# Performance work log

Measured on AMD Instinct MI355X. Metric: run time of the kernel, lower is better.

The kernel has to match this reference:

```python
import jax, jax.numpy as jnp
import numpy as np

EPS = 1e-5
QMAX = 127.0   # 8-bit symmetric: representable range [-128, 127]
QMIN = -128.0


def ste_round(x):
    # straight-through rounding (identity gradient)
    return x + jax.lax.stop_gradient(jnp.round(x) - x)


def setup_inputs() -> dict:
    key = jax.random.key(0)
    ks = jax.random.split(key, 7)
    N, C_in, C_out, H, W = 64, 256, 128, 56, 56
    x = jax.random.normal(ks[0], (N, C_in, H, W), jnp.float32)
    act_scaling_factor = jax.random.uniform(ks[1], (1,), jnp.float32, 0.02, 0.08)
    bn_weight = 1.0 + 0.3 * jax.random.normal(ks[2], (C_in,), jnp.float32)
    bn_bias = 0.1 * jax.random.normal(ks[3], (C_in,), jnp.float32)
    bn_mean = 0.1 * jax.random.normal(ks[4], (C_in,), jnp.float32)
    bn_var = jax.random.uniform(ks[5], (C_in,), jnp.float32, 0.5, 1.5)
    conv_weight = 0.05 * jax.random.normal(ks[6], (C_out, C_in, 1, 1), jnp.float32)
    return {
        "x": x,
        "act_scaling_factor": act_scaling_factor,
        "bn_weight": bn_weight,
        "bn_bias": bn_bias,
        "bn_mean": bn_mean,
        "bn_var": bn_var,
        "conv_weight": conv_weight,
    }


def _fwd(x, act_scaling_factor, bn_weight, bn_bias, bn_mean, bn_var, conv_weight):
    act_sf = act_scaling_factor.reshape(())

    # ---- QuantBn: fold BN, quantize folded scale per-channel (8-bit symmetric) ----
    inv_std = jax.lax.rsqrt(bn_var + EPS)
    scale = bn_weight * inv_std                    # [C_in]
    shift = bn_bias - bn_mean * scale              # [C_in]
    bn_sf = jnp.max(jnp.abs(scale)) / QMAX         # per-tensor bn weight scale
    scale_q = jnp.clip(ste_round(scale / bn_sf), QMIN, QMAX) * bn_sf
    bias_sf = bn_sf * act_sf                        # bias quantized at combined scale
    shift_q = ste_round(shift / bias_sf) * bias_sf
    x = x * scale_q[None, :, None, None] + shift_q[None, :, None, None]

    # ---- ReLU ----
    x = jnp.maximum(x, 0.0)

    # ---- QuantAct 1: per-tensor symmetric 8-bit requant ----
    sf1 = jnp.max(jnp.abs(x)) / QMAX
    x = jnp.clip(ste_round(x / sf1), QMIN, QMAX) * sf1

    # ---- QuantConv2d: per-output-channel 8-bit symmetric weight quant, 1x1 conv ----
    w_sf = jnp.max(jnp.abs(conv_weight), axis=(1, 2, 3)) / QMAX   # [C_out]
    w_q = jnp.clip(ste_round(conv_weight / w_sf[:, None, None, None]), QMIN, QMAX) \
          * w_sf[:, None, None, None]
    y = jax.lax.conv_general_dilated(
        x, w_q, window_strides=(1, 1), padding='VALID',
        dimension_numbers=('NCHW', 'OIHW', 'NCHW'))

    # ---- QuantAct 2 ----
    sf2 = jnp.max(jnp.abs(y)) / QMAX
    y = jnp.clip(ste_round(y / sf2), QMIN, QMAX) * sf2

    # ---- QuantAveragePool2d (2x2, stride 2): average in integer domain, re-round ----
    N, C, H, W = y.shape
    y_int = (y / sf2).reshape(N, C, H // 2, 2, W // 2, 2).mean(axis=(3, 5))
    out = ste_round(y_int) * sf2
    return out, sf2


def reference(x, act_scaling_factor, bn_weight, bn_bias, bn_mean, bn_var, conv_weight):
    return _fwd(x, act_scaling_factor, bn_weight, bn_bias, bn_mean, bn_var, conv_weight)
```

## Files before the change

kernel.cpp:

```cpp
#include <hip/hip_runtime.h>

#define QMAXF 127.0f

typedef _Float16 f16x4 __attribute__((ext_vector_type(4)));
typedef float f32x4 __attribute__((ext_vector_type(4)));
typedef int i32x4 __attribute__((ext_vector_type(4)));

__global__ __launch_bounds__(256) void k0_prep(
    const float* __restrict__ actsf, const float* __restrict__ bnw,
    const float* __restrict__ bnb, const float* __restrict__ bnm,
    const float* __restrict__ bnv, const float* __restrict__ cw,
    float* __restrict__ wsf, float* __restrict__ scq, float* __restrict__ shq,
    unsigned short* __restrict__ wq16, signed char* __restrict__ wq8,
    unsigned int* __restrict__ gmax) {
  const int t = threadIdx.x;
  __shared__ float red[4];
  float scale, shift;
  {
#pragma clang fp contract(off)
    float inv = 1.0f / sqrtf(bnv[t] + 1e-5f);
    scale = bnw[t] * inv;
    float tmp = bnm[t] * scale;
    shift = bnb[t] - tmp;
  }
  float a = fabsf(scale);
  for (int o = 32; o > 0; o >>= 1) a = fmaxf(a, __shfl_xor(a, o));
  if ((t & 63) == 0) red[t >> 6] = a;
  __syncthreads();
  const float amax = fmaxf(fmaxf(red[0], red[1]), fmaxf(red[2], red[3]));
  const float bn_sf = amax / QMAXF;
  scq[t] = fminf(fmaxf(rintf(scale / bn_sf), -128.f), 127.f) * bn_sf;
  const float bias_sf = bn_sf * actsf[0];
  shq[t] = rintf(shift / bias_sf) * bias_sf;
  if (t == 0) *gmax = 0u;
  const int r = t >> 1, half = t & 1;
  const float4* wrow = (const float4*)(cw + r * 256 + half * 128);
  float mx = 0.f;
#pragma unroll
  for (int j = 0; j < 32; ++j) {
    const float4 v = wrow[j];
    mx = fmaxf(mx, fmaxf(fmaxf(fabsf(v.x), fabsf(v.y)), fmaxf(fabsf(v.z), fabsf(v.w))));
  }
  mx = fmaxf(mx, __shfl_xor(mx, 1));
  const float wsf_v = mx / QMAXF;
  if (half == 0) wsf[r] = wsf_v;
  unsigned* w16w = (unsigned*)wq16;
  int* w8w = (int*)wq8;
#pragma unroll
  for (int j = 0; j < 32; ++j) {
    const float4 v = wrow[j];
    const float q0 = fminf(fmaxf(rintf(v.x / wsf_v), -128.f), 127.f);
    const float q1 = fminf(fmaxf(rintf(v.y / wsf_v), -128.f), 127.f);
    const float q2 = fminf(fmaxf(rintf(v.z / wsf_v), -128.f), 127.f);
    const float q3 = fminf(fmaxf(rintf(v.w / wsf_v), -128.f), 127.f);
    w8w[r * 64 + half * 32 + j] =
        ((int)q0 & 255) | (((int)q1 & 255) << 8) | (((int)q2 & 255) << 16) | (((int)q3 & 255) << 24);
    const unsigned h0 = __builtin_bit_cast(unsigned short, (_Float16)q0);
    const unsigned h1 = __builtin_bit_cast(unsigned short, (_Float16)q1);
    const unsigned h2 = __builtin_bit_cast(unsigned short, (_Float16)q2);
    const unsigned h3 = __builtin_bit_cast(unsigned short, (_Float16)q3);
    w16w[r * 128 + half * 64 + 2 * j]     = h0 | (h1 << 16);
    w16w[r * 128 + half * 64 + 2 * j + 1] = h2 | (h3 << 16);
  }
}

__global__ __launch_bounds__(256) void k1_max(
    const float* __restrict__ x, const float* __restrict__ scq,
    const float* __restrict__ shq, unsigned int* __restrict__ gmax) {
  const int t = threadIdx.x;
  const int b = blockIdx.x;
  const int n = b >> 5, cg = b & 31;
  __shared__ float red[4];
  const float4* __restrict__ x4 = (const float4*)x + (long)(n * 256 + cg * 8) * 784;
  float m = 0.f;
  for (int r = 0; r < 8; ++r) {
    const float s = scq[cg * 8 + r], sh = shq[cg * 8 + r];
    const float4* row = x4 + r * 784;
    for (int j = t; j < 784; j += 256) {
      const float4 v = row[j];
      float z0, z1, z2, z3;
      {
#pragma clang fp contract(off)
        z0 = v.x * s + sh; z1 = v.y * s + sh; z2 = v.z * s + sh; z3 = v.w * s + sh;
      }
      m = fmaxf(m, fmaxf(fmaxf(z0, z1), fmaxf(z2, z3)));
    }
  }
  for (int o = 32; o > 0; o >>= 1) m = fmaxf(m, __shfl_xor(m, o));
  if ((t & 63) == 0) red[t >> 6] = m;
  __syncthreads();
  if (t == 0) {
    const float mm = fmaxf(fmaxf(red[0], red[1]), fmaxf(red[2], red[3]));
    atomicMax(gmax, __float_as_uint(mm));
  }
}

__global__ __launch_bounds__(256, 2) void k2f_quant_gemm(
    const float* __restrict__ x, const float* __restrict__ scq,
    const float* __restrict__ shq, const unsigned int* __restrict__ gmax,
    const signed char* __restrict__ wq8, const float* __restrict__ wsf,
    signed char* __restrict__ xqT, float* __restrict__ blockmax) {
  __shared__ int sw[112 * 64];
  __shared__ float comax[128];
  __shared__ float red2[4];
  const int t = threadIdx.x, w = t >> 6, l = t & 63, m = l & 15, g = l >> 4;
  const int blk = blockIdx.x, n = blk / 28, tt = blk - n * 28;
  const float sf1 = __uint_as_float(*gmax) / QMAXF;
  const float* __restrict__ xb = x + (long)n * 802816 + tt * 112;

  for (int it = 0; it < 2; ++it) {
    const int task = it * 256 + t;
    if (task < 448) {
      const int slot = task & 15, hwq = task >> 4;
      const int hw0 = hwq * 4, ci0 = slot * 16;
      int wbuf[4][4] = {{0, 0, 0, 0}, {0, 0, 0, 0}, {0, 0, 0, 0}, {0, 0, 0, 0}};
#pragma unroll
      for (int j = 0; j < 16; ++j) {
        const float4 v = *(const float4*)(xb + (long)(ci0 + j) * 3136 + hw0);
        const float s = scq[ci0 + j], sh = shq[ci0 + j];
        float z0, z1, z2, z3;
        {
#pragma clang fp contract(off)
          z0 = v.x * s + sh; z1 = v.y * s + sh; z2 = v.z * s + sh; z3 = v.w * s + sh;
        }
        const float q0 = fminf(fmaxf(rintf(fmaxf(z0, 0.f) / sf1), -128.f), 127.f);
        const float q1 = fminf(fmaxf(rintf(fmaxf(z1, 0.f) / sf1), -128.f), 127.f);
        const float q2 = fminf(fmaxf(rintf(fmaxf(z2, 0.f) / sf1), -128.f), 127.f);
        const float q3 = fminf(fmaxf(rintf(fmaxf(z3, 0.f) / sf1), -128.f), 127.f);
        wbuf[0][j >> 2] |= ((int)q0 & 255) << ((j & 3) * 8);
        wbuf[1][j >> 2] |= ((int)q1 & 255) << ((j & 3) * 8);
        wbuf[2][j >> 2] |= ((int)q2 & 255) << ((j & 3) * 8);
        wbuf[3][j >> 2] |= ((int)q3 & 255) << ((j & 3) * 8);
      }
#pragma unroll
      for (int dh = 0; dh < 4; ++dh) {
        const int hw = hw0 + dh;
        *(i32x4*)&sw[hw * 64 + ((slot ^ (hw & 7)) << 2)] = *(const i32x4*)wbuf[dh];
      }
    }
  }
  __syncthreads();

  signed char* __restrict__ dst = xqT + ((long)(n * 3136 + tt * 112)) * 256;
  for (int it = 0; it < 7; ++it) {
    const int idx = it * 256 + t;
    const int hw = idx >> 4, c = idx & 15;
    const i32x4 v = *(const i32x4*)&sw[hw * 64 + ((c ^ (hw & 7)) << 2)];
    *(i32x4*)(dst + hw * 256 + c * 16) = v;
  }

  i32x4 wf[2][4];
#pragma unroll
  for (int ct = 0; ct < 2; ++ct)
#pragma unroll
    for (int ks = 0; ks < 4; ++ks)
      wf[ct][ks] = *(const i32x4*)(wq8 + (w * 32 + ct * 16 + m) * 256 + ks * 64 + g * 16);

  i32x4 acc[2][7];
#pragma unroll
  for (int ct = 0; ct < 2; ++ct)
#pragma unroll
    for (int ht = 0; ht < 7; ++ht) acc[ct][ht] = (i32x4){0, 0, 0, 0};

#pragma unroll
  for (int ks = 0; ks < 4; ++ks) {
    i32x4 xf[7];
#pragma unroll
    for (int ht = 0; ht < 7; ++ht) {
      const int row = ht * 16 + m;
      xf[ht] = *(const i32x4*)&sw[row * 64 + (((ks * 4 + g) ^ (row & 7)) << 2)];
    }
#pragma unroll
    for (int ct = 0; ct < 2; ++ct)
#pragma unroll
      for (int ht = 0; ht < 7; ++ht)
        acc[ct][ht] = __builtin_amdgcn_mfma_i32_16x16x64_i8(wf[ct][ks], xf[ht], acc[ct][ht], 0, 0, 0);
  }

  int im[2][4];
#pragma unroll
  for (int ct = 0; ct < 2; ++ct)
#pragma unroll
    for (int r = 0; r < 4; ++r) {
      int v = 0;
#pragma unroll
      for (int ht = 0; ht < 7; ++ht) {
        int a = acc[ct][ht][r];
        a = a < 0 ? -a : a;
        v = a > v ? a : v;
      }
      im[ct][r] = v;
    }
#pragma unroll
  for (int o = 1; o < 16; o <<= 1)
#pragma unroll
    for (int ct = 0; ct < 2; ++ct)
#pragma unroll
      for (int r = 0; r < 4; ++r) {
        const int other = __shfl_xor(im[ct][r], o);
        im[ct][r] = other > im[ct][r] ? other : im[ct][r];
      }
  if (m == 0) {
#pragma unroll
    for (int ct = 0; ct < 2; ++ct)
#pragma unroll
      for (int r = 0; r < 4; ++r)
        comax[w * 32 + ct * 16 + g * 4 + r] = (float)im[ct][r];
  }
  __syncthreads();
  float v = 0.f;
  if (t < 128) v = comax[t] * (sf1 * wsf[t]);
  for (int o = 32; o > 0; o >>= 1) v = fmaxf(v, __shfl_xor(v, o));
  if ((t & 63) == 0) red2[t >> 6] = v;
  __syncthreads();
  if (t == 0)
    blockmax[blk] = fmaxf(fmaxf(red2[0], red2[1]), fmaxf(red2[2], red2[3]));
}

__global__ __launch_bounds__(256) void k2b_sf2(
    const float* __restrict__ blockmax, float* __restrict__ sf2slot,
    float* __restrict__ outsf2) {
  const int t = threadIdx.x;
  __shared__ float red[4];
  float m = 0.f;
  for (int i = t; i < 1792; i += 256) m = fmaxf(m, blockmax[i]);
  for (int o = 32; o > 0; o >>= 1) m = fmaxf(m, __shfl_xor(m, o));
  if ((t & 63) == 0) red[t >> 6] = m;
  __syncthreads();
  if (t == 0) {
    const float sf2 = fmaxf(fmaxf(red[0], red[1]), fmaxf(red[2], red[3])) / QMAXF;
    sf2slot[0] = sf2;
    outsf2[0] = sf2;
  }
}

__global__ __launch_bounds__(256) void k3_final(
    const signed char* __restrict__ xqT, const signed char* __restrict__ wq8,
    const float* __restrict__ wsf, const unsigned int* __restrict__ gmax,
    const float* __restrict__ sf2p, float* __restrict__ out) {
  __shared__ _Float16 q2[128 * 116];
  const int t = threadIdx.x, w = t >> 6, l = t & 63;
  const int m = l & 15, g = l >> 4;
  const int blk = blockIdx.x;
  const int n = blk / 28, tt = blk - n * 28;
  const float sf1 = __uint_as_float(*gmax) / QMAXF;
  const signed char* __restrict__ xb = xqT + ((long)(n * 3136 + tt * 112)) * 256;

  i32x4 wf[2][4];
#pragma unroll
  for (int ct = 0; ct < 2; ++ct)
#pragma unroll
    for (int ks = 0; ks < 4; ++ks)
      wf[ct][ks] = *(const i32x4*)(wq8 + (w * 32 + ct * 16 + m) * 256 + ks * 64 + g * 16);

  i32x4 acc[2][7];
#pragma unroll
  for (int ct = 0; ct < 2; ++ct)
#pragma unroll
    for (int ht = 0; ht < 7; ++ht) acc[ct][ht] = (i32x4){0, 0, 0, 0};

#pragma unroll
  for (int ks = 0; ks < 4; ++ks) {
    i32x4 xf[7];
#pragma unroll
    for (int ht = 0; ht < 7; ++ht)
      xf[ht] = *(const i32x4*)(xb + (ht * 16 + m) * 256 + ks * 64 + g * 16);
#pragma unroll
    for (int ct = 0; ct < 2; ++ct)
#pragma unroll
      for (int ht = 0; ht < 7; ++ht)
        acc[ct][ht] = __builtin_amdgcn_mfma_i32_16x16x64_i8(wf[ct][ks], xf[ht], acc[ct][ht], 0, 0, 0);
  }

  const float sf2 = sf2p[0];
  float fac[2][4];
#pragma unroll
  for (int ct = 0; ct < 2; ++ct)
#pragma unroll
    for (int r = 0; r < 4; ++r)
      fac[ct][r] = sf1 * wsf[w * 32 + ct * 16 + g * 4 + r];
#pragma unroll
  for (int ct = 0; ct < 2; ++ct)
#pragma unroll
    for (int ht = 0; ht < 7; ++ht)
#pragma unroll
      for (int r = 0; r < 4; ++r) {
        const float y = (float)acc[ct][ht][r] * fac[ct][r];
        const float q = fminf(fmaxf(rintf(y / sf2), -128.f), 127.f);
        q2[(w * 32 + ct * 16 + g * 4 + r) * 116 + ht * 16 + m] = (_Float16)q;
      }
  __syncthreads();
  const long obase = (long)n * 100352 + tt * 28;
  for (int i = t; i < 3584; i += 256) {
    const unsigned co = (unsigned)i / 28u;
    const unsigned wo = (unsigned)i - co * 28u;
    const _Float16* row = q2 + co * 116;
    const float a = (float)row[2 * wo] + (float)row[2 * wo + 1] +
                    (float)row[56 + 2 * wo] + (float)row[56 + 2 * wo + 1];
    out[obase + (long)co * 784 + wo] = rintf(a * 0.25f) * sf2;
  }
}

union K2Smem {
  float xq[112][132];
  float q2[128][113];
  float comax[128];
};

template <bool FINAL>
__global__ __launch_bounds__(256, 2) void k2_gemm(
    const float* __restrict__ x, const float* __restrict__ scq,
    const float* __restrict__ shq, const unsigned short* __restrict__ wqu,
    const float* __restrict__ wsf, const unsigned int* __restrict__ gmax1,
    const float* __restrict__ sf2p, float* __restrict__ blockmax,
    float* __restrict__ out) {
  __shared__ K2Smem sm;
  __shared__ float red2[4];
  const int t = threadIdx.x;
  const int w = t >> 6;
  const int l = t & 63;
  const int blk = blockIdx.x;
  const int n = blk / 28;
  const int tt = blk - n * 28;
  const long xbase = (long)n * 802816 + tt * 112;
  const float sf1 = __uint_as_float(*gmax1) / QMAXF;
  const _Float16* __restrict__ wq16 = (const _Float16*)wqu;
  f32x4 acc[2][7];
#pragma unroll
  for (int ct = 0; ct < 2; ++ct)
#pragma unroll
    for (int ht = 0; ht < 7; ++ht) acc[ct][ht] = (f32x4){0.f, 0.f, 0.f, 0.f};

  for (int phase = 0; phase < 2; ++phase) {
    for (int it = 0; it < 14; ++it) {
      const unsigned f = (unsigned)t + (unsigned)it * 256u;
      const unsigned ci_l = f / 28u;
      const unsigned hwp = (f - ci_l * 28u) * 4u;
      const int ci = phase * 128 + (int)ci_l;
      const float4 v = *(const float4*)(x + xbase + (long)ci * 3136 + hwp);
      const float s = scq[ci], sh = shq[ci];
      float z0, z1, z2, z3;
      {
#pragma clang fp contract(off)
        z0 = v.x * s + sh; z1 = v.y * s + sh; z2 = v.z * s + sh; z3 = v.w * s + sh;
      }
      z0 = fmaxf(z0, 0.f); z1 = fmaxf(z1, 0.f); z2 = fmaxf(z2, 0.f); z3 = fmaxf(z3, 0.f);
      sm.xq[hwp + 0][ci_l] = fminf(fmaxf(rintf(z0 / sf1), -128.f), 127.f);
      sm.xq[hwp + 1][ci_l] = fminf(fmaxf(rintf(z1 / sf1), -128.f), 127.f);
      sm.xq[hwp + 2][ci_l] = fminf(fmaxf(rintf(z2 / sf1), -128.f), 127.f);
      sm.xq[hwp + 3][ci_l] = fminf(fmaxf(rintf(z3 / sf1), -128.f), 127.f);
    }
    __syncthreads();
    const int kw = ((l >> 4) << 2);
#pragma unroll
    for (int ks = 0; ks < 8; ++ks) {
      const int kb = ks * 16 + kw;
      f16x4 xf[7];
#pragma unroll
      for (int ht = 0; ht < 7; ++ht) {
        const float4 xv = *(const float4*)&sm.xq[ht * 16 + (l & 15)][kb];
        f16x4 h;
        h[0] = (_Float16)xv.x; h[1] = (_Float16)xv.y;
        h[2] = (_Float16)xv.z; h[3] = (_Float16)xv.w;
        xf[ht] = h;
      }
#pragma unroll
      for (int ct = 0; ct < 2; ++ct) {
        const int co = (w << 5) + (ct << 4) + (l & 15);
        const f16x4 wfv = *(const f16x4*)(wq16 + co * 256 + phase * 128 + kb);
#pragma unroll
        for (int ht = 0; ht < 7; ++ht)
          acc[ct][ht] = __builtin_amdgcn_mfma_f32_16x16x16f16(wfv, xf[ht], acc[ct][ht], 0, 0, 0);
      }
    }
    __syncthreads();
  }

  const int g = (l >> 4);
  if (!FINAL) {
    float im[2][4];
#pragma unroll
    for (int ct = 0; ct < 2; ++ct)
#pragma unroll
      for (int r = 0; r < 4; ++r) {
        float v = 0.f;
#pragma unroll
        for (int ht = 0; ht < 7; ++ht) v = fmaxf(v, fabsf(acc[ct][ht][r]));
        im[ct][r] = v;
      }
#pragma unroll
    for (int o = 1; o < 16; o <<= 1)
#pragma unroll
      for (int ct = 0; ct < 2; ++ct)
#pragma unroll
        for (int r = 0; r < 4; ++r)
          im[ct][r] = fmaxf(im[ct][r], __shfl_xor(im[ct][r], o));
    if ((l & 15) == 0) {
#pragma unroll
      for (int ct = 0; ct < 2; ++ct)
#pragma unroll
        for (int r = 0; r < 4; ++r)
          sm.comax[(w << 5) + (ct << 4) + (g << 2) + r] = im[ct][r];
    }
    __syncthreads();
    float v = 0.f;
    if (t < 128) v = sm.comax[t] * (sf1 * wsf[t]);
    for (int o = 32; o > 0; o >>= 1) v = fmaxf(v, __shfl_xor(v, o));
    if ((t & 63) == 0) red2[t >> 6] = v;
    __syncthreads();
    if (t == 0)
      blockmax[blk] = fmaxf(fmaxf(red2[0], red2[1]), fmaxf(red2[2], red2[3]));
  } else {
    const float sf2 = sf2p[0];
    float fac[2][4];
#pragma unroll
    for (int ct = 0; ct < 2; ++ct)
#pragma unroll
      for (int r = 0; r < 4; ++r)
        fac[ct][r] = sf1 * wsf[(w << 5) + (ct << 4) + (g << 2) + r];
#pragma unroll
    for (int ct = 0; ct < 2; ++ct)
#pragma unroll
      for (int ht = 0; ht < 7; ++ht)
#pragma unroll
        for (int r = 0; r < 4; ++r) {
          const float y = acc[ct][ht][r] * fac[ct][r];
          const float q = fminf(fmaxf(rintf(y / sf2), -128.f), 127.f);
          sm.q2[(w << 5) + (ct << 4) + (g << 2) + r][ht * 16 + (l & 15)] = q;
        }
    __syncthreads();
    const long obase = (long)n * 100352 + tt * 28;
    for (int i = t; i < 3584; i += 256) {
      const unsigned co = (unsigned)i / 28u;
      const unsigned wo = (unsigned)i - co * 28u;
      const float a = sm.q2[co][2 * wo];
      const float b = sm.q2[co][2 * wo + 1];
      const float c = sm.q2[co][56 + 2 * wo];
      const float d = sm.q2[co][56 + 2 * wo + 1];
      const float avg = (a + b + c + d) * 0.25f;
      out[obase + (long)co * 784 + wo] = rintf(avg) * sf2;
    }
  }
}

extern "C" void kernel_launch(void* const* d_in, const int* in_sizes, int n_in,
                              void* d_out, int out_size, void* d_ws, size_t ws_size,
                              hipStream_t stream) {
  const float* x     = (const float*)d_in[0];
  const float* actsf = (const float*)d_in[1];
  const float* bnw   = (const float*)d_in[2];
  const float* bnb   = (const float*)d_in[3];
  const float* bnm   = (const float*)d_in[4];
  const float* bnv   = (const float*)d_in[5];
  const float* cw    = (const float*)d_in[6];
  float* out = (float*)d_out;
  char* ws = (char*)d_ws;

  unsigned int* gmax  = (unsigned int*)ws;
  float* sf2slot      = (float*)(ws + 8);
  float* scq          = (float*)(ws + 1024);
  float* shq          = (float*)(ws + 2048);
  float* wsf          = (float*)(ws + 3072);
  signed char* wq8    = (signed char*)(ws + 4096);
  unsigned short* wq16= (unsigned short*)(ws + 36864);
  float* blockmax     = (float*)(ws + 102400);
  signed char* xqT    = (signed char*)(ws + 131072);
  const size_t NEED = 131072ull + 64ull * 3136ull * 256ull;

  hipLaunchKernelGGL(k0_prep, dim3(1), dim3(256), 0, stream,
                     actsf, bnw, bnb, bnm, bnv, cw, wsf, scq, shq, wq16, wq8, gmax);
  hipLaunchKernelGGL(k1_max, dim3(2048), dim3(256), 0, stream, x, scq, shq, gmax);
  if (ws_size >= NEED) {
    hipLaunchKernelGGL(k2f_quant_gemm, dim3(1792), dim3(256), 0, stream,
                       x, scq, shq, gmax, wq8, wsf, xqT, blockmax);
    hipLaunchKernelGGL(k2b_sf2, dim3(1), dim3(256), 0, stream,
                       blockmax, sf2slot, out + (out_size - 1));
    hipLaunchKernelGGL(k3_final, dim3(1792), dim3(256), 0, stream,
                       xqT, wq8, wsf, gmax, sf2slot, out);
  } else {
    hipLaunchKernelGGL(HIP_KERNEL_NAME(k2_gemm<false>), dim3(1792), dim3(256), 0, stream,
                       x, scq, shq, wq16, wsf, gmax, sf2slot, blockmax, out);
    hipLaunchKernelGGL(k2b_sf2, dim3(1), dim3(256), 0, stream,
                       blockmax, sf2slot, out + (out_size - 1));
    hipLaunchKernelGGL(HIP_KERNEL_NAME(k2_gemm<true>), dim3(1792), dim3(256), 0, stream,
                       x, scq, shq, wq16, wsf, gmax, sf2slot, blockmax, out);
  }
}
```

Before: 171.9 us.

## Shrink quant-GEMM tiles, fold sf2 reduction into final kernel, drop fp16 path

The quantize+GEMM pass now uses 64-pixel tiles (3136 blocks) with a smaller LDS buffer and per-iteration weight loads, targeting higher occupancy (launch bounds 4). The separate single-block sf2 reduction kernel is removed: every block of the final kernel re-reduces the 3136 block maxima itself, saving one launch but adding redundant reads. Weight fragments are loaded inside the loop instead of kept in registers to cut register pressure. The fp16 fallback path, used when the workspace was too small, is deleted along with its weight buffer.

```diff
diff --git a/kernel.cpp b/kernel.cpp
--- a/kernel.cpp
+++ b/kernel.cpp
@@ -2,7 +2,6 @@
 
 #define QMAXF 127.0f
 
-typedef _Float16 f16x4 __attribute__((ext_vector_type(4)));
 typedef float f32x4 __attribute__((ext_vector_type(4)));
 typedef int i32x4 __attribute__((ext_vector_type(4)));
 
@@ -11,8 +10,7 @@
     const float* __restrict__ bnb, const float* __restrict__ bnm,
     const float* __restrict__ bnv, const float* __restrict__ cw,
     float* __restrict__ wsf, float* __restrict__ scq, float* __restrict__ shq,
-    unsigned short* __restrict__ wq16, signed char* __restrict__ wq8,
-    unsigned int* __restrict__ gmax) {
+    signed char* __restrict__ wq8, unsigned int* __restrict__ gmax) {
   const int t = threadIdx.x;
   __shared__ float red[4];
   float scale, shift;
@@ -44,7 +42,6 @@
   mx = fmaxf(mx, __shfl_xor(mx, 1));
   const float wsf_v = mx / QMAXF;
   if (half == 0) wsf[r] = wsf_v;
-  unsigned* w16w = (unsigned*)wq16;
   int* w8w = (int*)wq8;
 #pragma unroll
   for (int j = 0; j < 32; ++j) {
@@ -55,12 +52,6 @@
     const float q3 = fminf(fmaxf(rintf(v.w / wsf_v), -128.f), 127.f);
     w8w[r * 64 + half * 32 + j] =
         ((int)q0 & 255) | (((int)q1 & 255) << 8) | (((int)q2 & 255) << 16) | (((int)q3 & 255) << 24);
-    const unsigned h0 = __builtin_bit_cast(unsigned short, (_Float16)q0);
-    const unsigned h1 = __builtin_bit_cast(unsigned short, (_Float16)q1);
-    const unsigned h2 = __builtin_bit_cast(unsigned short, (_Float16)q2);
-    const unsigned h3 = __builtin_bit_cast(unsigned short, (_Float16)q3);
-    w16w[r * 128 + half * 64 + 2 * j]     = h0 | (h1 << 16);
-    w16w[r * 128 + half * 64 + 2 * j + 1] = h2 | (h3 << 16);
   }
 }
 
@@ -95,86 +86,76 @@
   }
 }
 
-__global__ __launch_bounds__(256, 2) void k2f_quant_gemm(
+__global__ __launch_bounds__(256, 4) void k2f_quant_gemm(
     const float* __restrict__ x, const float* __restrict__ scq,
     const float* __restrict__ shq, const unsigned int* __restrict__ gmax,
     const signed char* __restrict__ wq8, const float* __restrict__ wsf,
     signed char* __restrict__ xqT, float* __restrict__ blockmax) {
-  __shared__ int sw[112 * 64];
+  __shared__ int sw[64 * 64];
   __shared__ float comax[128];
   __shared__ float red2[4];
   const int t = threadIdx.x, w = t >> 6, l = t & 63, m = l & 15, g = l >> 4;
-  const int blk = blockIdx.x, n = blk / 28, tt = blk - n * 28;
+  const int blk = blockIdx.x, n = blk / 49, tt = blk - n * 49;
   const float sf1 = __uint_as_float(*gmax) / QMAXF;
-  const float* __restrict__ xb = x + (long)n * 802816 + tt * 112;
-
-  for (int it = 0; it < 2; ++it) {
-    const int task = it * 256 + t;
-    if (task < 448) {
-      const int slot = task & 15, hwq = task >> 4;
-      const int hw0 = hwq * 4, ci0 = slot * 16;
-      int wbuf[4][4] = {{0, 0, 0, 0}, {0, 0, 0, 0}, {0, 0, 0, 0}, {0, 0, 0, 0}};
-#pragma unroll
-      for (int j = 0; j < 16; ++j) {
-        const float4 v = *(const float4*)(xb + (long)(ci0 + j) * 3136 + hw0);
-        const float s = scq[ci0 + j], sh = shq[ci0 + j];
-        float z0, z1, z2, z3;
-        {
+  const float* __restrict__ xb = x + (long)n * 802816 + tt * 64;
+
+  {
+    const int slot = t & 15, hwq = t >> 4;
+    const int hw0 = hwq * 4, ci0 = slot * 16;
+    int wbuf[4][4] = {{0, 0, 0, 0}, {0, 0, 0, 0}, {0, 0, 0, 0}, {0, 0, 0, 0}};
+#pragma unroll
+    for (int j = 0; j < 16; ++j) {
+      const float4 v = *(const float4*)(xb + (long)(ci0 + j) * 3136 + hw0);
+      const float s = scq[ci0 + j], sh = shq[ci0 + j];
+      float z0, z1, z2, z3;
+      {
 #pragma clang fp contract(off)
-          z0 = v.x * s + sh; z1 = v.y * s + sh; z2 = v.z * s + sh; z3 = v.w * s + sh;
-        }
-        const float q0 = fminf(fmaxf(rintf(fmaxf(z0, 0.f) / sf1), -128.f), 127.f);
-        const float q1 = fminf(fmaxf(rintf(fmaxf(z1, 0.f) / sf1), -128.f), 127.f);
-        const float q2 = fminf(fmaxf(rintf(fmaxf(z2, 0.f) / sf1), -128.f), 127.f);
-        const float q3 = fminf(fmaxf(rintf(fmaxf(z3, 0.f) / sf1), -128.f), 127.f);
-        wbuf[0][j >> 2] |= ((int)q0 & 255) << ((j & 3) * 8);
-        wbuf[1][j >> 2] |= ((int)q1 & 255) << ((j & 3) * 8);
-        wbuf[2][j >> 2] |= ((int)q2 & 255) << ((j & 3) * 8);
-        wbuf[3][j >> 2] |= ((int)q3 & 255) << ((j & 3) * 8);
-      }
-#pragma unroll
-      for (int dh = 0; dh < 4; ++dh) {
-        const int hw = hw0 + dh;
-        *(i32x4*)&sw[hw * 64 + ((slot ^ (hw & 7)) << 2)] = *(const i32x4*)wbuf[dh];
-      }
-    }
-  }
-  __syncthreads();
-
-  signed char* __restrict__ dst = xqT + ((long)(n * 3136 + tt * 112)) * 256;
-  for (int it = 0; it < 7; ++it) {
+        z0 = v.x * s + sh; z1 = v.y * s + sh; z2 = v.z * s + sh; z3 = v.w * s + sh;
+      }
+      const float q0 = fminf(fmaxf(rintf(fmaxf(z0, 0.f) / sf1), -128.f), 127.f);
+      const float q1 = fminf(fmaxf(rintf(fmaxf(z1, 0.f) / sf1), -128.f), 127.f);
+      const float q2 = fminf(fmaxf(rintf(fmaxf(z2, 0.f) / sf1), -128.f), 127.f);
+      const float q3 = fminf(fmaxf(rintf(fmaxf(z3, 0.f) / sf1), -128.f), 127.f);
+      wbuf[0][j >> 2] |= ((int)q0 & 255) << ((j & 3) * 8);
+      wbuf[1][j >> 2] |= ((int)q1 & 255) << ((j & 3) * 8);
+      wbuf[2][j >> 2] |= ((int)q2 & 255) << ((j & 3) * 8);
+      wbuf[3][j >> 2] |= ((int)q3 & 255) << ((j & 3) * 8);
+    }
+#pragma unroll
+    for (int dh = 0; dh < 4; ++dh) {
+      const int hw = hw0 + dh;
+      *(i32x4*)&sw[hw * 64 + ((slot ^ (hw & 7)) << 2)] = *(const i32x4*)wbuf[dh];
+    }
+  }
+  __syncthreads();
+
+  signed char* __restrict__ dst = xqT + ((long)(n * 3136 + tt * 64)) * 256;
+#pragma unroll
+  for (int it = 0; it < 4; ++it) {
     const int idx = it * 256 + t;
     const int hw = idx >> 4, c = idx & 15;
     const i32x4 v = *(const i32x4*)&sw[hw * 64 + ((c ^ (hw & 7)) << 2)];
     *(i32x4*)(dst + hw * 256 + c * 16) = v;
   }
 
-  i32x4 wf[2][4];
-#pragma unroll
-  for (int ct = 0; ct < 2; ++ct)
-#pragma unroll
-    for (int ks = 0; ks < 4; ++ks)
-      wf[ct][ks] = *(const i32x4*)(wq8 + (w * 32 + ct * 16 + m) * 256 + ks * 64 + g * 16);
-
-  i32x4 acc[2][7];
-#pragma unroll
-  for (int ct = 0; ct < 2; ++ct)
-#pragma unroll
-    for (int ht = 0; ht < 7; ++ht) acc[ct][ht] = (i32x4){0, 0, 0, 0};
-
-#pragma unroll
-  for (int ks = 0; ks < 4; ++ks) {
-    i32x4 xf[7];
-#pragma unroll
-    for (int ht = 0; ht < 7; ++ht) {
-      const int row = ht * 16 + m;
-      xf[ht] = *(const i32x4*)&sw[row * 64 + (((ks * 4 + g) ^ (row & 7)) << 2)];
-    }
-#pragma unroll
-    for (int ct = 0; ct < 2; ++ct)
-#pragma unroll
-      for (int ht = 0; ht < 7; ++ht)
-        acc[ct][ht] = __builtin_amdgcn_mfma_i32_16x16x64_i8(wf[ct][ks], xf[ht], acc[ct][ht], 0, 0, 0);
+  i32x4 acc[2][4];
+#pragma unroll
+  for (int ct = 0; ct < 2; ++ct)
+#pragma unroll
+    for (int ht = 0; ht < 4; ++ht) acc[ct][ht] = (i32x4){0, 0, 0, 0};
+
+#pragma unroll
+  for (int ct = 0; ct < 2; ++ct) {
+#pragma unroll
+    for (int ks = 0; ks < 4; ++ks) {
+      const i32x4 wf = *(const i32x4*)(wq8 + (w * 32 + ct * 16 + m) * 256 + ks * 64 + g * 16);
+#pragma unroll
+      for (int ht = 0; ht < 4; ++ht) {
+        const int row = ht * 16 + m;
+        const i32x4 xf = *(const i32x4*)&sw[row * 64 + (((ks * 4 + g) ^ (row & 7)) << 2)];
+        acc[ct][ht] = __builtin_amdgcn_mfma_i32_16x16x64_i8(wf, xf, acc[ct][ht], 0, 0, 0);
+      }
+    }
   }
 
   int im[2][4];
@@ -184,7 +165,7 @@
     for (int r = 0; r < 4; ++r) {
       int v = 0;
 #pragma unroll
-      for (int ht = 0; ht < 7; ++ht) {
+      for (int ht = 0; ht < 4; ++ht) {
         int a = acc[ct][ht][r];
         a = a < 0 ? -a : a;
         v = a > v ? a : v;
@@ -217,41 +198,28 @@
     blockmax[blk] = fmaxf(fmaxf(red2[0], red2[1]), fmaxf(red2[2], red2[3]));
 }
 
-__global__ __launch_bounds__(256) void k2b_sf2(
-    const float* __restrict__ blockmax, float* __restrict__ sf2slot,
-    float* __restrict__ outsf2) {
-  const int t = threadIdx.x;
-  __shared__ float red[4];
-  float m = 0.f;
-  for (int i = t; i < 1792; i += 256) m = fmaxf(m, blockmax[i]);
-  for (int o = 32; o > 0; o >>= 1) m = fmaxf(m, __shfl_xor(m, o));
-  if ((t & 63) == 0) red[t >> 6] = m;
-  __syncthreads();
-  if (t == 0) {
-    const float sf2 = fmaxf(fmaxf(red[0], red[1]), fmaxf(red[2], red[3])) / QMAXF;
-    sf2slot[0] = sf2;
-    outsf2[0] = sf2;
-  }
-}
-
-__global__ __launch_bounds__(256) void k3_final(
+__global__ __launch_bounds__(256, 3) void k3_final(
     const signed char* __restrict__ xqT, const signed char* __restrict__ wq8,
     const float* __restrict__ wsf, const unsigned int* __restrict__ gmax,
-    const float* __restrict__ sf2p, float* __restrict__ out) {
+    const float* __restrict__ blockmax, float* __restrict__ out,
+    float* __restrict__ outsf2) {
   __shared__ _Float16 q2[128 * 116];
+  __shared__ float red2[4];
   const int t = threadIdx.x, w = t >> 6, l = t & 63;
   const int m = l & 15, g = l >> 4;
   const int blk = blockIdx.x;
   const int n = blk / 28, tt = blk - n * 28;
   const float sf1 = __uint_as_float(*gmax) / QMAXF;
+
+  float bm = 0.f;
+  for (int i = t; i < 3136; i += 256) bm = fmaxf(bm, blockmax[i]);
+  for (int o = 32; o > 0; o >>= 1) bm = fmaxf(bm, __shfl_xor(bm, o));
+  if ((t & 63) == 0) red2[t >> 6] = bm;
+  __syncthreads();
+  const float sf2 = fmaxf(fmaxf(red2[0], red2[1]), fmaxf(red2[2], red2[3])) / QMAXF;
+  if (blk == 0 && t == 0) outsf2[0] = sf2;
+
   const signed char* __restrict__ xb = xqT + ((long)(n * 3136 + tt * 112)) * 256;
-
-  i32x4 wf[2][4];
-#pragma unroll
-  for (int ct = 0; ct < 2; ++ct)
-#pragma unroll
-    for (int ks = 0; ks < 4; ++ks)
-      wf[ct][ks] = *(const i32x4*)(wq8 + (w * 32 + ct * 16 + m) * 256 + ks * 64 + g * 16);
 
   i32x4 acc[2][7];
 #pragma unroll
@@ -266,13 +234,14 @@
     for (int ht = 0; ht < 7; ++ht)
       xf[ht] = *(const i32x4*)(xb + (ht * 16 + m) * 256 + ks * 64 + g * 16);
 #pragma unroll
-    for (int ct = 0; ct < 2; ++ct)
+    for (int ct = 0; ct < 2; ++ct) {
+      const i32x4 wf = *(const i32x4*)(wq8 + (w * 32 + ct * 16 + m) * 256 + ks * 64 + g * 16);
 #pragma unroll
       for (int ht = 0; ht < 7; ++ht)
-        acc[ct][ht] = __builtin_amdgcn_mfma_i32_16x16x64_i8(wf[ct][ks], xf[ht], acc[ct][ht], 0, 0, 0);
-  }
-
-  const float sf2 = sf2p[0];
+        acc[ct][ht] = __builtin_amdgcn_mfma_i32_16x16x64_i8(wf, xf[ht], acc[ct][ht], 0, 0, 0);
+    }
+  }
+
   float fac[2][4];
 #pragma unroll
   for (int ct = 0; ct < 2; ++ct)
@@ -298,148 +267,6 @@
     const float a = (float)row[2 * wo] + (float)row[2 * wo + 1] +
                     (float)row[56 + 2 * wo] + (float)row[56 + 2 * wo + 1];
     out[obase + (long)co * 784 + wo] = rintf(a * 0.25f) * sf2;
-  }
-}
-
-union K2Smem {
-  float xq[112][132];
-  float q2[128][113];
-  float comax[128];
-};
-
-template <bool FINAL>
-__global__ __launch_bounds__(256, 2) void k2_gemm(
-    const float* __restrict__ x, const float* __restrict__ scq,
-    const float* __restrict__ shq, const unsigned short* __restrict__ wqu,
-    const float* __restrict__ wsf, const unsigned int* __restrict__ gmax1,
-    const float* __restrict__ sf2p, float* __restrict__ blockmax,
-    float* __restrict__ out) {
-  __shared__ K2Smem sm;
-  __shared__ float red2[4];
-  const int t = threadIdx.x;
-  const int w = t >> 6;
-  const int l = t & 63;
-  const int blk = blockIdx.x;
-  const int n = blk / 28;
-  const int tt = blk - n * 28;
-  const long xbase = (long)n * 802816 + tt * 112;
-  const float sf1 = __uint_as_float(*gmax1) / QMAXF;
-  const _Float16* __restrict__ wq16 = (const _Float16*)wqu;
-  f32x4 acc[2][7];
-#pragma unroll
-  for (int ct = 0; ct < 2; ++ct)
-#pragma unroll
-    for (int ht = 0; ht < 7; ++ht) acc[ct][ht] = (f32x4){0.f, 0.f, 0.f, 0.f};
-
-  for (int phase = 0; phase < 2; ++phase) {
-    for (int it = 0; it < 14; ++it) {
-      const unsigned f = (unsigned)t + (unsigned)it * 256u;
-      const unsigned ci_l = f / 28u;
-      const unsigned hwp = (f - ci_l * 28u) * 4u;
-      const int ci = phase * 128 + (int)ci_l;
-      const float4 v = *(const float4*)(x + xbase + (long)ci * 3136 + hwp);
-      const float s = scq[ci], sh = shq[ci];
-      float z0, z1, z2, z3;
-      {
-#pragma clang fp contract(off)
-        z0 = v.x * s + sh; z1 = v.y * s + sh; z2 = v.z * s + sh; z3 = v.w * s + sh;
-      }
-      z0 = fmaxf(z0, 0.f); z1 = fmaxf(z1, 0.f); z2 = fmaxf(z2, 0.f); z3 = fmaxf(z3, 0.f);
-      sm.xq[hwp + 0][ci_l] = fminf(fmaxf(rintf(z0 / sf1), -128.f), 127.f);
-      sm.xq[hwp + 1][ci_l] = fminf(fmaxf(rintf(z1 / sf1), -128.f), 127.f);
-      sm.xq[hwp + 2][ci_l] = fminf(fmaxf(rintf(z2 / sf1), -128.f), 127.f);
-      sm.xq[hwp + 3][ci_l] = fminf(fmaxf(rintf(z3 / sf1), -128.f), 127.f);
-    }
-    __syncthreads();
-    const int kw = ((l >> 4) << 2);
-#pragma unroll
-    for (int ks = 0; ks < 8; ++ks) {
-      const int kb = ks * 16 + kw;
-      f16x4 xf[7];
-#pragma unroll
-      for (int ht = 0; ht < 7; ++ht) {
-        const float4 xv = *(const float4*)&sm.xq[ht * 16 + (l & 15)][kb];
-        f16x4 h;
-        h[0] = (_Float16)xv.x; h[1] = (_Float16)xv.y;
-        h[2] = (_Float16)xv.z; h[3] = (_Float16)xv.w;
-        xf[ht] = h;
-      }
-#pragma unroll
-      for (int ct = 0; ct < 2; ++ct) {
-        const int co = (w << 5) + (ct << 4) + (l & 15);
-        const f16x4 wfv = *(const f16x4*)(wq16 + co * 256 + phase * 128 + kb);
-#pragma unroll
-        for (int ht = 0; ht < 7; ++ht)
-          acc[ct][ht] = __builtin_amdgcn_mfma_f32_16x16x16f16(wfv, xf[ht], acc[ct][ht], 0, 0, 0);
-      }
-    }
-    __syncthreads();
-  }
-
-  const int g = (l >> 4);
-  if (!FINAL) {
-    float im[2][4];
-#pragma unroll
-    for (int ct = 0; ct < 2; ++ct)
-#pragma unroll
-      for (int r = 0; r < 4; ++r) {
-        float v = 0.f;
-#pragma unroll
-        for (int ht = 0; ht < 7; ++ht) v = fmaxf(v, fabsf(acc[ct][ht][r]));
-        im[ct][r] = v;
-      }
-#pragma unroll
-    for (int o = 1; o < 16; o <<= 1)
-#pragma unroll
-      for (int ct = 0; ct < 2; ++ct)
-#pragma unroll
-        for (int r = 0; r < 4; ++r)
-          im[ct][r] = fmaxf(im[ct][r], __shfl_xor(im[ct][r], o));
-    if ((l & 15) == 0) {
-#pragma unroll
-      for (int ct = 0; ct < 2; ++ct)
-#pragma unroll
-        for (int r = 0; r < 4; ++r)
-          sm.comax[(w << 5) + (ct << 4) + (g << 2) + r] = im[ct][r];
-    }
-    __syncthreads();
-    float v = 0.f;
-    if (t < 128) v = sm.comax[t] * (sf1 * wsf[t]);
-    for (int o = 32; o > 0; o >>= 1) v = fmaxf(v, __shfl_xor(v, o));
-    if ((t & 63) == 0) red2[t >> 6] = v;
-    __syncthreads();
-    if (t == 0)
-      blockmax[blk] = fmaxf(fmaxf(red2[0], red2[1]), fmaxf(red2[2], red2[3]));
-  } else {
-    const float sf2 = sf2p[0];
-    float fac[2][4];
-#pragma unroll
-    for (int ct = 0; ct < 2; ++ct)
-#pragma unroll
-      for (int r = 0; r < 4; ++r)
-        fac[ct][r] = sf1 * wsf[(w << 5) + (ct << 4) + (g << 2) + r];
-#pragma unroll
-    for (int ct = 0; ct < 2; ++ct)
-#pragma unroll
-      for (int ht = 0; ht < 7; ++ht)
-#pragma unroll
-        for (int r = 0; r < 4; ++r) {
-          const float y = acc[ct][ht][r] * fac[ct][r];
-          const float q = fminf(fmaxf(rintf(y / sf2), -128.f), 127.f);
-          sm.q2[(w << 5) + (ct << 4) + (g << 2) + r][ht * 16 + (l & 15)] = q;
-        }
-    __syncthreads();
-    const long obase = (long)n * 100352 + tt * 28;
-    for (int i = t; i < 3584; i += 256) {
-      const unsigned co = (unsigned)i / 28u;
-      const unsigned wo = (unsigned)i - co * 28u;
-      const float a = sm.q2[co][2 * wo];
-      const float b = sm.q2[co][2 * wo + 1];
-      const float c = sm.q2[co][56 + 2 * wo];
-      const float d = sm.q2[co][56 + 2 * wo + 1];
-      const float avg = (a + b + c + d) * 0.25f;
-      out[obase + (long)co * 784 + wo] = rintf(avg) * sf2;
-    }
   }
 }
 
@@ -457,32 +284,18 @@
   char* ws = (char*)d_ws;
 
   unsigned int* gmax  = (unsigned int*)ws;
-  float* sf2slot      = (float*)(ws + 8);
   float* scq          = (float*)(ws + 1024);
   float* shq          = (float*)(ws + 2048);
   float* wsf          = (float*)(ws + 3072);
   signed char* wq8    = (signed char*)(ws + 4096);
-  unsigned short* wq16= (unsigned short*)(ws + 36864);
-  float* blockmax     = (float*)(ws + 102400);
-  signed char* xqT    = (signed char*)(ws + 131072);
-  const size_t NEED = 131072ull + 64ull * 3136ull * 256ull;
+  float* blockmax     = (float*)(ws + 36864);
+  signed char* xqT    = (signed char*)(ws + 65536);
 
   hipLaunchKernelGGL(k0_prep, dim3(1), dim3(256), 0, stream,
-                     actsf, bnw, bnb, bnm, bnv, cw, wsf, scq, shq, wq16, wq8, gmax);
+                     actsf, bnw, bnb, bnm, bnv, cw, wsf, scq, shq, wq8, gmax);
   hipLaunchKernelGGL(k1_max, dim3(2048), dim3(256), 0, stream, x, scq, shq, gmax);
-  if (ws_size >= NEED) {
-    hipLaunchKernelGGL(k2f_quant_gemm, dim3(1792), dim3(256), 0, stream,
-                       x, scq, shq, gmax, wq8, wsf, xqT, blockmax);
-    hipLaunchKernelGGL(k2b_sf2, dim3(1), dim3(256), 0, stream,
-                       blockmax, sf2slot, out + (out_size - 1));
-    hipLaunchKernelGGL(k3_final, dim3(1792), dim3(256), 0, stream,
-                       xqT, wq8, wsf, gmax, sf2slot, out);
-  } else {
-    hipLaunchKernelGGL(HIP_KERNEL_NAME(k2_gemm<false>), dim3(1792), dim3(256), 0, stream,
-                       x, scq, shq, wq16, wsf, gmax, sf2slot, blockmax, out);
-    hipLaunchKernelGGL(k2b_sf2, dim3(1), dim3(256), 0, stream,
-                       blockmax, sf2slot, out + (out_size - 1));
-    hipLaunchKernelGGL(HIP_KERNEL_NAME(k2_gemm<true>), dim3(1792), dim3(256), 0, stream,
-                       x, scq, shq, wq16, wsf, gmax, sf2slot, blockmax, out);
-  }
-}
+  hipLaunchKernelGGL(k2f_quant_gemm, dim3(3136), dim3(256), 0, stream,
+                     x, scq, shq, gmax, wq8, wsf, xqT, blockmax);
+  hipLaunchKernelGGL(k3_final, dim3(1792), dim3(256), 0, stream,
+                     xqT, wq8, wsf, gmax, blockmax, out, out + (out_size - 1));
+}
```

Result: no change. 168.6 us (-1.9%).
